# Kernel optimization log

Measured on AMD Instinct MI355X. Metric: run time of the kernel, lower is better.

## Reference

```python
import jax, jax.numpy as jnp
from jax import lax
import numpy as np

KS = 15  # kernel_size
PAD = KS // 2


def setup_inputs() -> dict:
    key = jax.random.key(0)
    k1, _ = jax.random.split(key)
    images = jax.random.uniform(k1, (16, 3, 1024, 1024), dtype=jnp.float32)
    # uniform box filter weight, matches conv.weight.fill_(1/(k*k))
    weight = jnp.ones((1, 1, KS, KS), dtype=jnp.float32)
    return {"images": images, "weight": weight}


def reference(images, weight):
    # channel-wise min over B, G, R channels -> [B, 1, H, W]
    dark = jnp.min(images[:, :3, :, :], axis=1, keepdims=True)
    # 15x15 box average conv, padding=7, no bias
    w = weight * (1.0 / (KS * KS))
    out = lax.conv_general_dilated(
        dark, w,
        window_strides=(1, 1),
        padding=[(PAD, PAD), (PAD, PAD)],
        dimension_numbers=("NCHW", "OIHW", "NCHW"),
    )
    return out
```

## Files before the change

kernel.cpp:

```cpp
#include <hip/hip_runtime.h>

#define KS   15
#define PAD  7
#define TILE 64
#define HI   (TILE + KS - 1)
#define LDW  84
#define NQ   20

__global__ __launch_bounds__(256, 6) void dcp_kernel(
    const float* __restrict__ img, const float* __restrict__ weight,
    float* __restrict__ out)
{
    __shared__ float S[HI * LDW];

    const int tid  = threadIdx.x;
    const int wave = tid >> 6;
    const int lane = tid & 63;

    const int bid = blockIdx.x;
    const int swz = (bid & 7) * 512 + (bid >> 3);
    const int b   = swz >> 8;
    const int ty0 = ((swz >> 4) & 15) * TILE;
    const int tx0 = (swz & 15) * TILE;

    const int H = 1024, W = 1024;
    const long long plane = (long long)H * W;
    const float* base = img + (long long)b * 3 * plane;
    const float scale = weight[0] * (1.0f / (KS * KS));

    for (int it = tid; it < HI * NQ; it += 256) {
        const int r  = it / NQ;
        const int c4 = it - r * NQ;
        const int gy = ty0 + r - PAD;
        const int gx = tx0 - 8 + 4 * c4;
        float4 v = make_float4(0.f, 0.f, 0.f, 0.f);
        if ((unsigned)gy < (unsigned)H && (unsigned)gx <= (unsigned)(W - 4)) {
            const long long off = (long long)gy * W + gx;
            const float4 a0 = *(const float4*)(base + off);
            const float4 a1 = *(const float4*)(base + off + plane);
            const float4 a2 = *(const float4*)(base + off + 2 * plane);
            v.x = fminf(a0.x, fminf(a1.x, a2.x));
            v.y = fminf(a0.y, fminf(a1.y, a2.y));
            v.z = fminf(a0.z, fminf(a1.z, a2.z));
            v.w = fminf(a0.w, fminf(a1.w, a2.w));
        }
        *(float4*)(&S[r * LDW + 4 * c4]) = v;
    }
    __syncthreads();

    float buf[32] __attribute__((aligned(16)));

    {
        const int rb = wave * 16;
        #pragma unroll
        for (int k = 0; k < 30; ++k) buf[k] = S[(rb + k) * LDW + lane];
        __syncthreads();
        float run = 0.f;
        #pragma unroll
        for (int k = 0; k < 14; ++k) run += buf[k];
        #pragma unroll
        for (int j = 0; j < 16; ++j) {
            run += buf[j + 14];
            S[(rb + j) * LDW + lane] = run;
            run -= buf[j];
        }
    }
    {
        const int rb = wave * 16;
        const int c  = 64 + lane;
        if (lane < 16) {
            #pragma unroll
            for (int k = 0; k < 30; ++k) buf[k] = S[(rb + k) * LDW + c];
        }
        __syncthreads();
        if (lane < 16) {
            float run = 0.f;
            #pragma unroll
            for (int k = 0; k < 14; ++k) run += buf[k];
            #pragma unroll
            for (int j = 0; j < 16; ++j) {
                run += buf[j + 14];
                S[(rb + j) * LDW + c] = run;
                run -= buf[j];
            }
        }
        __syncthreads();
    }

    {
        const int r = lane;
        const int s = wave;
        const int bp = r * LDW + s * 16;
        #pragma unroll
        for (int q = 0; q < 8; ++q)
            *(float4*)(&buf[4 * q]) = *(const float4*)(&S[bp + 4 * q]);
        float o[16];
        float run = 0.f;
        #pragma unroll
        for (int k = 1; k <= 14; ++k) run += buf[k];
        #pragma unroll
        for (int j = 0; j < 16; ++j) {
            run += buf[j + 15];
            o[j] = run * scale;
            run -= buf[j + 1];
        }
        float* dst = out + (long long)b * plane + (long long)(ty0 + r) * W + (tx0 + s * 16);
        #pragma unroll
        for (int q = 0; q < 4; ++q)
            *(float4*)(dst + 4 * q) =
                make_float4(o[4 * q], o[4 * q + 1], o[4 * q + 2], o[4 * q + 3]);
    }
}

extern "C" void kernel_launch(void* const* d_in, const int* in_sizes, int n_in,
                              void* d_out, int out_size, void* d_ws, size_t ws_size,
                              hipStream_t stream) {
    const float* img    = (const float*)d_in[0];
    const float* weight = (const float*)d_in[1];
    float* out = (float*)d_out;

    dim3 grid(4096);
    dim3 block(256);
    dcp_kernel<<<grid, block, 0, stream>>>(img, weight, out);
}
```

Baseline: 58.83 us.

## Software-pipeline tile loads and stage output through LDS for coalesced stores

The input load loop is unrolled with a register double buffer, so the three channel loads for the next iteration are issued before the current min is written to LDS. The output is no longer stored directly from each thread's 16-column strip, which gives strided row-per-lane writes. It is written to LDS with stride 68 and then copied out as fully coalesced float4 rows. The cost is extra registers, which may reduce occupancy, plus extra barriers and an LDS round trip.

```diff
diff --git a/kernel.cpp b/kernel.cpp
--- a/kernel.cpp
+++ b/kernel.cpp
@@ -6,6 +6,8 @@
 #define HI   (TILE + KS - 1)
 #define LDW  84
 #define NQ   20
+#define NIT  (HI * NQ)
+#define STR2 68
 
 __global__ __launch_bounds__(256, 6) void dcp_kernel(
     const float* __restrict__ img, const float* __restrict__ weight,
@@ -28,23 +30,45 @@
     const float* base = img + (long long)b * 3 * plane;
     const float scale = weight[0] * (1.0f / (KS * KS));
 
-    for (int it = tid; it < HI * NQ; it += 256) {
-        const int r  = it / NQ;
-        const int c4 = it - r * NQ;
-        const int gy = ty0 + r - PAD;
-        const int gx = tx0 - 8 + 4 * c4;
-        float4 v = make_float4(0.f, 0.f, 0.f, 0.f);
+    auto load3 = [&](int it, float4* c) {
+        int r  = it / NQ;
+        int c4 = it - r * NQ;
+        int gy = ty0 + r - PAD;
+        int gx = tx0 - 8 + 4 * c4;
         if ((unsigned)gy < (unsigned)H && (unsigned)gx <= (unsigned)(W - 4)) {
-            const long long off = (long long)gy * W + gx;
-            const float4 a0 = *(const float4*)(base + off);
-            const float4 a1 = *(const float4*)(base + off + plane);
-            const float4 a2 = *(const float4*)(base + off + 2 * plane);
-            v.x = fminf(a0.x, fminf(a1.x, a2.x));
-            v.y = fminf(a0.y, fminf(a1.y, a2.y));
-            v.z = fminf(a0.z, fminf(a1.z, a2.z));
-            v.w = fminf(a0.w, fminf(a1.w, a2.w));
+            long long off = (long long)gy * W + gx;
+            c[0] = *(const float4*)(base + off);
+            c[1] = *(const float4*)(base + off + plane);
+            c[2] = *(const float4*)(base + off + 2 * plane);
+        } else {
+            c[0] = c[1] = c[2] = make_float4(0.f, 0.f, 0.f, 0.f);
         }
+    };
+    auto write_min = [&](int it, const float4* c) {
+        int r  = it / NQ;
+        int c4 = it - r * NQ;
+        float4 v;
+        v.x = fminf(c[0].x, fminf(c[1].x, c[2].x));
+        v.y = fminf(c[0].y, fminf(c[1].y, c[2].y));
+        v.z = fminf(c[0].z, fminf(c[1].z, c[2].z));
+        v.w = fminf(c[0].w, fminf(c[1].w, c[2].w));
         *(float4*)(&S[r * LDW + 4 * c4]) = v;
+    };
+
+    {
+        float4 c0[3], c1[3];
+        load3(tid, c0);
+        #pragma unroll
+        for (int k = 0; k < 5; ++k) {
+            load3(tid + 256 * (k + 1), c1);
+            write_min(tid + 256 * k, c0);
+            c0[0] = c1[0]; c0[1] = c1[1]; c0[2] = c1[2];
+        }
+        write_min(tid + 256 * 5, c0);
+        if (tid < NIT - 1536) {
+            load3(1536 + tid, c0);
+            write_min(1536 + tid, c0);
+        }
     }
     __syncthreads();
 
@@ -104,11 +128,24 @@
             o[j] = run * scale;
             run -= buf[j + 1];
         }
-        float* dst = out + (long long)b * plane + (long long)(ty0 + r) * W + (tx0 + s * 16);
+        __syncthreads();
         #pragma unroll
         for (int q = 0; q < 4; ++q)
-            *(float4*)(dst + 4 * q) =
+            *(float4*)(&S[r * STR2 + s * 16 + 4 * q]) =
                 make_float4(o[4 * q], o[4 * q + 1], o[4 * q + 2], o[4 * q + 3]);
+    }
+    __syncthreads();
+
+    {
+        float* obase = out + (long long)b * plane + (long long)ty0 * W + tx0;
+        #pragma unroll
+        for (int k = 0; k < 4; ++k) {
+            const int qi  = tid + 256 * k;
+            const int row = qi >> 4;
+            const int qc  = qi & 15;
+            float4 v = *(const float4*)(&S[row * STR2 + 4 * qc]);
+            *(float4*)(obase + (long long)row * W + 4 * qc) = v;
+        }
     }
 }
 
```

After: 53.33 us. 1.1x faster.
